# Kernel tuning notes

Measured on AMD Instinct MI355X. Metric: run time of the kernel, lower is better.

The kernel has to match this reference:

```python
import jax, jax.numpy as jnp
import numpy as np
from jax import lax

EPS = 1e-5

def _groupnorm1(v, scale, bias):
    # GroupNorm(1, C) on [bs, C] vectors (spatial dims are 1x1): normalize over C per sample
    m = jnp.mean(v, axis=-1, keepdims=True)
    var = jnp.mean((v - m) ** 2, axis=-1, keepdims=True)
    return (v - m) / jnp.sqrt(var + EPS) * scale + bias

def _mish(v):
    return v * jnp.tanh(jax.nn.softplus(v))


def setup_inputs() -> dict:
    key = jax.random.key(0)
    ks = jax.random.split(key, 5)
    bs, C, H, W = 32, 128, 64, 64
    K, red = 4, 16
    hid = C // red
    return {
        "x": jax.random.normal(ks[0], (bs, C, H, W), jnp.float32),
        "weight": jax.random.normal(ks[1], (K, C, C, 3, 3), jnp.float32) * 0.05,
        "bias": jax.random.normal(ks[2], (K, C), jnp.float32) * 0.05,
        "se_w1": jax.random.normal(ks[3], (hid, C), jnp.float32) * 0.1,
        "gn1_scale": jnp.ones((hid,), jnp.float32),
        "gn1_bias": jnp.zeros((hid,), jnp.float32),
        "se_w2": jax.random.normal(ks[4], (K, hid), jnp.float32) * 0.1,
        "gn2_scale": jnp.ones((K,), jnp.float32),
        "gn2_bias": jnp.zeros((K,), jnp.float32),
    }


def reference(x, weight, bias, se_w1, gn1_scale, gn1_bias, se_w2, gn2_scale, gn2_bias):
    bs, C, H, W = x.shape
    K, out_p, in_p, kh, kw = weight.shape

    # --- SqueezeAndExcitation attention -> [bs, K] in (0,1) ---
    pooled = jnp.mean(x, axis=(2, 3))                       # [bs, C]
    h1 = pooled @ se_w1.T                                   # [bs, hid] (1x1 conv, no bias)
    h1 = _mish(_groupnorm1(h1, gn1_scale, gn1_bias))
    h2 = h1 @ se_w2.T                                       # [bs, K]
    att = jax.nn.sigmoid(_groupnorm1(h2, gn2_scale, gn2_bias))

    # --- per-sample kernel / bias aggregation ---
    agg_w = jnp.einsum('bk,koihw->boihw', att, weight)      # [bs, out, in, kh, kw]
    agg_b = att @ bias                                      # [bs, out]

    # --- per-sample conv2d (equivalent to groups=bs grouped conv in torch) ---
    pad = ((1, 1), (1, 1))
    def per_sample(xi, wi):
        return lax.conv_general_dilated(
            xi[None], wi, window_strides=(1, 1), padding=pad,
            dimension_numbers=('NCHW', 'OIHW', 'NCHW'))[0]
    out = jax.vmap(per_sample)(x, agg_w)                    # [bs, out, H, W]
    return out + agg_b[:, :, None, None]
```

## Files before the change

### kernel.cpp

```cpp
#include <hip/hip_runtime.h>
#include <hip/hip_bf16.h>
#include <math.h>
#include <stdint.h>

#define EPS 1e-5f

typedef __attribute__((ext_vector_type(8))) short bf16x8;
typedef __attribute__((ext_vector_type(16))) float f32x16;

__device__ __forceinline__ ushort f2bf(float f) {
    union { float f; unsigned u; } v; v.f = f;
    unsigned r = (v.u + 0x7FFFu + ((v.u >> 16) & 1u)) >> 16;
    return (ushort)r;
}

__device__ __forceinline__ void dma16(const void* g, void* l) {
    __builtin_amdgcn_global_load_lds(
        (__attribute__((address_space(1))) const void*)(uintptr_t)g,
        (__attribute__((address_space(3))) void*)(uintptr_t)l,
        16, 0, 0);
}

__global__ __launch_bounds__(256) void transpose_kernel(const float* __restrict__ x,
                                                        ushort* __restrict__ xT,
                                                        float* __restrict__ partial) {
    __shared__ float T2[64][132];
    int bid = blockIdx.x;
    int b = (bid & 7) * 4 + (bid >> 9);
    int y = (bid >> 3) & 63;
    int t = threadIdx.x;

    int ic2 = t >> 1, half = t & 1;
    const float4* src = (const float4*)(x + (((size_t)b * 128 + ic2) * 64 + y) * 64 + half * 32);
    float s = 0.f;
#pragma unroll
    for (int i = 0; i < 8; ++i) {
        float4 v = src[i];
        int c0 = half * 32 + i * 4;
        T2[c0][ic2] = v.x; T2[c0 + 1][ic2] = v.y; T2[c0 + 2][ic2] = v.z; T2[c0 + 3][ic2] = v.w;
        s += v.x + v.y + v.z + v.w;
    }
    s += __shfl_xor(s, 1, 64);
    if (half == 0) partial[((size_t)b * 64 + y) * 128 + ic2] = s;
    __syncthreads();

    int col = t >> 2, icq = t & 3;
    const float4* row = (const float4*)&T2[col][icq * 32];
    uint pk[16];
#pragma unroll
    for (int m = 0; m < 8; ++m) {
        float4 v = row[m];
        pk[2 * m]     = (uint)f2bf(v.x) | ((uint)f2bf(v.y) << 16);
        pk[2 * m + 1] = (uint)f2bf(v.z) | ((uint)f2bf(v.w) << 16);
    }
    ushort* dst = xT + (((size_t)(b * 66 + y + 1)) * 66 + col + 1) * 128 + icq * 32;
    ((uint4*)dst)[0] = make_uint4(pk[0], pk[1], pk[2], pk[3]);
    ((uint4*)dst)[1] = make_uint4(pk[4], pk[5], pk[6], pk[7]);
    ((uint4*)dst)[2] = make_uint4(pk[8], pk[9], pk[10], pk[11]);
    ((uint4*)dst)[3] = make_uint4(pk[12], pk[13], pk[14], pk[15]);

    uint4 z = make_uint4(0, 0, 0, 0);
    if (y == 0) {
        uint4* row0 = (uint4*)(xT + ((size_t)b * 66 + 0) * 66 * 128);
        for (int i = t; i < 1056; i += 256) row0[i] = z;
    }
    if (y == 63) {
        uint4* row65 = (uint4*)(xT + ((size_t)b * 66 + 65) * 66 * 128);
        for (int i = t; i < 1056; i += 256) row65[i] = z;
    }
    if (t < 32) {
        int c = (t >> 4) * 65;
        int i = t & 15;
        *(uint4*)(xT + (((size_t)(b * 66 + y + 1)) * 66 + c) * 128 + i * 8) = z;
    }
}

__global__ __launch_bounds__(256) void sefuse_kernel(const float* __restrict__ partial,
                                                     const float* __restrict__ se_w1,
                                                     const float* __restrict__ gn1_s, const float* __restrict__ gn1_b,
                                                     const float* __restrict__ se_w2,
                                                     const float* __restrict__ gn2_s, const float* __restrict__ gn2_b,
                                                     float* __restrict__ att) {
    __shared__ float sA[256];
    __shared__ float pl[128];
    __shared__ float h1s[8];
    int b = blockIdx.x;
    int t = threadIdx.x;
    int ic = t & 127, hf = t >> 7;

    const float* p = partial + ((size_t)b * 64 + hf * 32) * 128 + ic;
    float s = 0.f;
#pragma unroll
    for (int k = 0; k < 32; ++k) s += p[k * 128];
    sA[t] = s;
    __syncthreads();
    if (t < 128) pl[t] = (sA[t] + sA[t + 128]) * (1.0f / 4096.0f);
    __syncthreads();
    if (t < 8) {
        float s1 = 0.f;
        for (int c = 0; c < 128; ++c) s1 += pl[c] * se_w1[t * 128 + c];
        h1s[t] = s1;
    }
    __syncthreads();
    if (t == 0) {
        float h1[8];
#pragma unroll
        for (int j = 0; j < 8; ++j) h1[j] = h1s[j];
        float m = 0.f;
#pragma unroll
        for (int j = 0; j < 8; ++j) m += h1[j];
        m *= 0.125f;
        float var = 0.f;
#pragma unroll
        for (int j = 0; j < 8; ++j) { float d = h1[j] - m; var += d * d; }
        var *= 0.125f;
        float inv = rsqrtf(var + EPS);
#pragma unroll
        for (int j = 0; j < 8; ++j) {
            float tt = (h1[j] - m) * inv * gn1_s[j] + gn1_b[j];
            float sp = (tt > 20.f) ? tt : log1pf(expf(tt));
            h1[j] = tt * tanhf(sp);
        }
        float h2[4];
#pragma unroll
        for (int k = 0; k < 4; ++k) {
            float s2 = 0.f;
#pragma unroll
            for (int j = 0; j < 8; ++j) s2 += h1[j] * se_w2[k * 8 + j];
            h2[k] = s2;
        }
        float m2 = 0.25f * (h2[0] + h2[1] + h2[2] + h2[3]);
        float v2 = 0.f;
#pragma unroll
        for (int k = 0; k < 4; ++k) { float d = h2[k] - m2; v2 += d * d; }
        v2 *= 0.25f;
        float inv2 = rsqrtf(v2 + EPS);
#pragma unroll
        for (int k = 0; k < 4; ++k) {
            float tt = (h2[k] - m2) * inv2 * gn2_s[k] + gn2_b[k];
            att[b * 4 + k] = 1.0f / (1.0f + expf(-tt));
        }
    }
}

__global__ __launch_bounds__(256) void aggw_kernel(const float* __restrict__ weight,
                                                   const float* __restrict__ att,
                                                   ushort* __restrict__ aggw) {
    int tq = (blockIdx.x % 72) * 256 + threadIdx.x;
    int rep = blockIdx.x / 72;
    int tap = tq >> 10;
    int within = tq & 1023;
    int oc = within >> 3;
    int p = within & 7;
    int g = (p - oc) & 7;
    int h = tap / 9, s = tap % 9;
    int ic0 = h * 64 + g * 8;

    float wv[4][8];
#pragma unroll
    for (int k = 0; k < 4; ++k)
#pragma unroll
        for (int j = 0; j < 8; ++j)
            wv[k][j] = weight[(((size_t)(k * 128 + oc)) * 128 + ic0 + j) * 9 + s];

    for (int b = rep * 8; b < rep * 8 + 8; ++b) {
        float a0 = att[b * 4 + 0], a1 = att[b * 4 + 1], a2 = att[b * 4 + 2], a3 = att[b * 4 + 3];
        uint pk[4];
#pragma unroll
        for (int q = 0; q < 4; ++q) {
            float f0 = a0 * wv[0][2 * q] + a1 * wv[1][2 * q] + a2 * wv[2][2 * q] + a3 * wv[3][2 * q];
            float f1 = a0 * wv[0][2 * q + 1] + a1 * wv[1][2 * q + 1] + a2 * wv[2][2 * q + 1] + a3 * wv[3][2 * q + 1];
            pk[q] = (uint)f2bf(f0) | ((uint)f2bf(f1) << 16);
        }
        *(uint4*)(aggw + (size_t)b * 147456 + (size_t)tq * 8) = make_uint4(pk[0], pk[1], pk[2], pk[3]);
    }
}

__global__ __launch_bounds__(512, 4) void conv_kernel(const ushort* __restrict__ xT,
                                                      const ushort* __restrict__ aggw,
                                                      const float* __restrict__ att,
                                                      const float* __restrict__ bias,
                                                      float* __restrict__ out) {
    __shared__ ushort ldsB[396 * 64];

    int bid = blockIdx.x;
    int xcd = bid & 7;
    int idx = bid >> 3;
    int b = xcd * 4 + (idx >> 4);
    int tile = idx & 15;
    int y0 = tile * 4;

    int tid = threadIdx.x;
    int l = tid & 63, w = tid >> 6;
    int wm = w & 1, wn = w >> 1;
    int l31 = l & 31, lhi = l >> 5;

    const ushort* xTb = xT + ((size_t)(b * 66 + y0)) * 66 * 128;
    const ushort* Asmp = aggw + (size_t)b * 147456;

    int ocofs[2], rotA[2];
#pragma unroll
    for (int mi = 0; mi < 2; ++mi) {
        int oc = wm * 64 + mi * 32 + l31;
        ocofs[mi] = oc * 64;
        rotA[mi] = (lhi + oc) & 7;
    }
    int CB[2];
#pragma unroll
    for (int ch = 0; ch < 2; ++ch) CB[ch] = wn * 66 + ch * 32 + l31;
    int rotB = (l31 + lhi) & 7;

    f32x16 acc[2][2];
#pragma unroll
    for (int mi = 0; mi < 2; ++mi)
#pragma unroll
        for (int ch = 0; ch < 2; ++ch)
#pragma unroll
            for (int q = 0; q < 16; ++q) acc[mi][ch][q] = 0.f;

    bf16x8 a[2][4];
#pragma unroll
    for (int mi = 0; mi < 2; ++mi)
#pragma unroll
        for (int icb = 0; icb < 4; ++icb)
            a[mi][icb] = *(const bf16x8*)(Asmp + ocofs[mi] + (((rotA[mi] + 2 * icb) & 7) << 3));

#pragma unroll
    for (int i = 0; i < 7; ++i) {
        int k = i * 512 + tid;
        if (k < 3168) {
            int rc = k >> 3;
            int c = rc % 66;
            int g = ((k & 7) - c) & 7;
            dma16(xTb + (size_t)rc * 128 + (g << 3), &ldsB[(size_t)k * 8]);
        }
    }
    __syncthreads();

    for (int hs = 0; hs < 18; ++hs) {
        int s = (hs >= 9) ? hs - 9 : hs;
        int kh = s / 3, kw = s - kh * 3;
        int celladd = kh * 66 + kw;
        const ushort* Anext = Asmp + (size_t)(hs + 1) * 8192;
#pragma unroll
        for (int icb = 0; icb < 4; ++icb) {
            int slotb = (rotB + 2 * icb + kw) & 7;
            bf16x8 bb[2];
#pragma unroll
            for (int ch = 0; ch < 2; ++ch) {
                int cell = CB[ch] + celladd;
                bb[ch] = *(const bf16x8*)&ldsB[(cell << 6) + (slotb << 3)];
            }
#pragma unroll
            for (int mi = 0; mi < 2; ++mi)
#pragma unroll
                for (int ch = 0; ch < 2; ++ch)
                    acc[mi][ch] = __builtin_amdgcn_mfma_f32_32x32x16_bf16(a[mi][icb], bb[ch], acc[mi][ch], 0, 0, 0);
            if (hs < 17) {
#pragma unroll
                for (int mi = 0; mi < 2; ++mi)
                    a[mi][icb] = *(const bf16x8*)(Anext + ocofs[mi] + (((rotA[mi] + 2 * icb) & 7) << 3));
            }
        }
        if (hs == 8) {
            __syncthreads();
#pragma unroll
            for (int i = 0; i < 7; ++i) {
                int k = i * 512 + tid;
                if (k < 3168) {
                    int rc = k >> 3;
                    int c = rc % 66;
                    int g = ((k & 7) - c) & 7;
                    dma16(xTb + (size_t)rc * 128 + 64 + (g << 3), &ldsB[(size_t)k * 8]);
                }
            }
            __syncthreads();
        }
    }

    float a0 = att[b * 4 + 0], a1 = att[b * 4 + 1], a2 = att[b * 4 + 2], a3 = att[b * 4 + 3];
    int y = y0 + wn;
#pragma unroll
    for (int mi = 0; mi < 2; ++mi)
#pragma unroll
        for (int q = 0; q < 16; ++q) {
            int oc = wm * 64 + mi * 32 + (q & 3) + 8 * (q >> 2) + 4 * lhi;
            float ab = a0 * bias[oc] + a1 * bias[128 + oc] + a2 * bias[256 + oc] + a3 * bias[384 + oc];
#pragma unroll
            for (int ch = 0; ch < 2; ++ch)
                out[(((size_t)b * 128 + oc) * 64 + y) * 64 + ch * 32 + l31] = acc[mi][ch][q] + ab;
        }
}

extern "C" void kernel_launch(void* const* d_in, const int* in_sizes, int n_in,
                              void* d_out, int out_size, void* d_ws, size_t ws_size,
                              hipStream_t stream) {
    const float* x      = (const float*)d_in[0];
    const float* weight = (const float*)d_in[1];
    const float* bias   = (const float*)d_in[2];
    const float* se_w1  = (const float*)d_in[3];
    const float* gn1_s  = (const float*)d_in[4];
    const float* gn1_b  = (const float*)d_in[5];
    const float* se_w2  = (const float*)d_in[6];
    const float* gn2_s  = (const float*)d_in[7];
    const float* gn2_b  = (const float*)d_in[8];
    float* out = (float*)d_out;

    float*  att     = (float*)((char*)d_ws + 16384);
    float*  partial = (float*)((char*)d_ws + 65536);
    ushort* aggw    = (ushort*)((char*)d_ws + 65536);
    ushort* xT      = (ushort*)((char*)d_ws + 10485760);

    transpose_kernel<<<2048, 256, 0, stream>>>(x, xT, partial);
    sefuse_kernel<<<32, 256, 0, stream>>>(partial, se_w1, gn1_s, gn1_b, se_w2, gn2_s, gn2_b, att);
    aggw_kernel<<<288, 256, 0, stream>>>(weight, att, aggw);
    conv_kernel<<<512, 512, 0, stream>>>(xT, aggw, att, bias, out);
}
```

Measured before the change: 105.0 us.

## Fuse SE path into aggregation kernel and enlarge conv tile to eight rows

Spatial pooling now uses atomic adds into a zeroed pooled buffer, replacing the per-row partial sums. Each aggregation block recomputes the squeeze-and-excitation attention for its eight samples, which removes the separate SE kernel launch. The conv kernel tile grows from four to eight output rows per block: each wave computes four N-subtiles instead of two, LDS use grows, and the grid halves to 256 blocks. In exchange this adds atomic contention, redundant SE computation and a memset, and the larger tile lowers occupancy and leaves fewer blocks than before to spread across CUs.

```diff
diff --git a/kernel.cpp b/kernel.cpp
--- a/kernel.cpp
+++ b/kernel.cpp
@@ -23,7 +23,7 @@
 
 __global__ __launch_bounds__(256) void transpose_kernel(const float* __restrict__ x,
                                                         ushort* __restrict__ xT,
-                                                        float* __restrict__ partial) {
+                                                        float* __restrict__ pooled) {
     __shared__ float T2[64][132];
     int bid = blockIdx.x;
     int b = (bid & 7) * 4 + (bid >> 9);
@@ -41,7 +41,7 @@
         s += v.x + v.y + v.z + v.w;
     }
     s += __shfl_xor(s, 1, 64);
-    if (half == 0) partial[((size_t)b * 64 + y) * 128 + ic2] = s;
+    if (half == 0) atomicAdd(&pooled[b * 128 + ic2], s * (1.0f / 4096.0f));
     __syncthreads();
 
     int col = t >> 2, icq = t & 3;
@@ -75,37 +75,39 @@
     }
 }
 
-__global__ __launch_bounds__(256) void sefuse_kernel(const float* __restrict__ partial,
-                                                     const float* __restrict__ se_w1,
-                                                     const float* __restrict__ gn1_s, const float* __restrict__ gn1_b,
-                                                     const float* __restrict__ se_w2,
-                                                     const float* __restrict__ gn2_s, const float* __restrict__ gn2_b,
-                                                     float* __restrict__ att) {
-    __shared__ float sA[256];
-    __shared__ float pl[128];
-    __shared__ float h1s[8];
-    int b = blockIdx.x;
+__global__ __launch_bounds__(256) void aggw_kernel(const float* __restrict__ weight,
+                                                   const float* __restrict__ pooled,
+                                                   const float* __restrict__ se_w1,
+                                                   const float* __restrict__ gn1_s, const float* __restrict__ gn1_b,
+                                                   const float* __restrict__ se_w2,
+                                                   const float* __restrict__ gn2_s, const float* __restrict__ gn2_b,
+                                                   float* __restrict__ att_out,
+                                                   ushort* __restrict__ aggw) {
+    __shared__ float pl[8][128];
+    __shared__ float h1s[8][8];
+    __shared__ float att_s[8][4];
+    int blk = blockIdx.x;
+    int rep = blk / 72;
     int t = threadIdx.x;
-    int ic = t & 127, hf = t >> 7;
-
-    const float* p = partial + ((size_t)b * 64 + hf * 32) * 128 + ic;
-    float s = 0.f;
-#pragma unroll
-    for (int k = 0; k < 32; ++k) s += p[k * 128];
-    sA[t] = s;
-    __syncthreads();
-    if (t < 128) pl[t] = (sA[t] + sA[t + 128]) * (1.0f / 4096.0f);
+
+#pragma unroll
+    for (int u = 0; u < 4; ++u) {
+        int pid = u * 256 + t;
+        int bl = pid >> 7, ic = pid & 127;
+        pl[bl][ic] = pooled[(rep * 8 + bl) * 128 + ic];
+    }
+    __syncthreads();
+    if (t < 64) {
+        int bl = t >> 3, jj = t & 7;
+        float s1 = 0.f;
+        for (int c = 0; c < 128; ++c) s1 += pl[bl][c] * se_w1[jj * 128 + c];
+        h1s[bl][jj] = s1;
+    }
     __syncthreads();
     if (t < 8) {
-        float s1 = 0.f;
-        for (int c = 0; c < 128; ++c) s1 += pl[c] * se_w1[t * 128 + c];
-        h1s[t] = s1;
-    }
-    __syncthreads();
-    if (t == 0) {
         float h1[8];
 #pragma unroll
-        for (int j = 0; j < 8; ++j) h1[j] = h1s[j];
+        for (int j = 0; j < 8; ++j) h1[j] = h1s[t][j];
         float m = 0.f;
 #pragma unroll
         for (int j = 0; j < 8; ++j) m += h1[j];
@@ -138,16 +140,14 @@
 #pragma unroll
         for (int k = 0; k < 4; ++k) {
             float tt = (h2[k] - m2) * inv2 * gn2_s[k] + gn2_b[k];
-            att[b * 4 + k] = 1.0f / (1.0f + expf(-tt));
-        }
-    }
-}
-
-__global__ __launch_bounds__(256) void aggw_kernel(const float* __restrict__ weight,
-                                                   const float* __restrict__ att,
-                                                   ushort* __restrict__ aggw) {
-    int tq = (blockIdx.x % 72) * 256 + threadIdx.x;
-    int rep = blockIdx.x / 72;
+            att_s[t][k] = 1.0f / (1.0f + expf(-tt));
+        }
+    }
+    __syncthreads();
+
+    if ((blk % 72) == 0 && t < 32) att_out[rep * 32 + t] = att_s[t >> 2][t & 3];
+
+    int tq = (blk % 72) * 256 + t;
     int tap = tq >> 10;
     int within = tq & 1023;
     int oc = within >> 3;
@@ -163,8 +163,10 @@
         for (int j = 0; j < 8; ++j)
             wv[k][j] = weight[(((size_t)(k * 128 + oc)) * 128 + ic0 + j) * 9 + s];
 
-    for (int b = rep * 8; b < rep * 8 + 8; ++b) {
-        float a0 = att[b * 4 + 0], a1 = att[b * 4 + 1], a2 = att[b * 4 + 2], a3 = att[b * 4 + 3];
+#pragma unroll
+    for (int bl = 0; bl < 8; ++bl) {
+        int b = rep * 8 + bl;
+        float a0 = att_s[bl][0], a1 = att_s[bl][1], a2 = att_s[bl][2], a3 = att_s[bl][3];
         uint pk[4];
 #pragma unroll
         for (int q = 0; q < 4; ++q) {
@@ -176,23 +178,23 @@
     }
 }
 
-__global__ __launch_bounds__(512, 4) void conv_kernel(const ushort* __restrict__ xT,
+__global__ __launch_bounds__(512, 2) void conv_kernel(const ushort* __restrict__ xT,
                                                       const ushort* __restrict__ aggw,
                                                       const float* __restrict__ att,
                                                       const float* __restrict__ bias,
                                                       float* __restrict__ out) {
-    __shared__ ushort ldsB[396 * 64];
+    __shared__ ushort ldsB[660 * 64];
 
     int bid = blockIdx.x;
     int xcd = bid & 7;
-    int idx = bid >> 3;
-    int b = xcd * 4 + (idx >> 4);
-    int tile = idx & 15;
-    int y0 = tile * 4;
+    int j = bid >> 3;
+    int b = xcd * 4 + (j >> 3);
+    int tile = j & 7;
+    int y0 = tile * 8;
 
     int tid = threadIdx.x;
     int l = tid & 63, w = tid >> 6;
-    int wm = w & 1, wn = w >> 1;
+    int wm = w >> 2, wn = w & 3;
     int l31 = l & 31, lhi = l >> 5;
 
     const ushort* xTb = xT + ((size_t)(b * 66 + y0)) * 66 * 128;
@@ -205,18 +207,19 @@
         ocofs[mi] = oc * 64;
         rotA[mi] = (lhi + oc) & 7;
     }
-    int CB[2];
-#pragma unroll
-    for (int ch = 0; ch < 2; ++ch) CB[ch] = wn * 66 + ch * 32 + l31;
+    int CB[4];
+#pragma unroll
+    for (int nb = 0; nb < 4; ++nb)
+        CB[nb] = (2 * wn + (nb >> 1)) * 66 + (nb & 1) * 32 + l31;
     int rotB = (l31 + lhi) & 7;
 
-    f32x16 acc[2][2];
+    f32x16 acc[2][4];
 #pragma unroll
     for (int mi = 0; mi < 2; ++mi)
 #pragma unroll
-        for (int ch = 0; ch < 2; ++ch)
-#pragma unroll
-            for (int q = 0; q < 16; ++q) acc[mi][ch][q] = 0.f;
+        for (int nb = 0; nb < 4; ++nb)
+#pragma unroll
+            for (int q = 0; q < 16; ++q) acc[mi][nb][q] = 0.f;
 
     bf16x8 a[2][4];
 #pragma unroll
@@ -226,9 +229,9 @@
             a[mi][icb] = *(const bf16x8*)(Asmp + ocofs[mi] + (((rotA[mi] + 2 * icb) & 7) << 3));
 
 #pragma unroll
-    for (int i = 0; i < 7; ++i) {
+    for (int i = 0; i < 11; ++i) {
         int k = i * 512 + tid;
-        if (k < 3168) {
+        if (k < 5280) {
             int rc = k >> 3;
             int c = rc % 66;
             int g = ((k & 7) - c) & 7;
@@ -245,17 +248,17 @@
 #pragma unroll
         for (int icb = 0; icb < 4; ++icb) {
             int slotb = (rotB + 2 * icb + kw) & 7;
-            bf16x8 bb[2];
-#pragma unroll
-            for (int ch = 0; ch < 2; ++ch) {
-                int cell = CB[ch] + celladd;
-                bb[ch] = *(const bf16x8*)&ldsB[(cell << 6) + (slotb << 3)];
+            bf16x8 bb[4];
+#pragma unroll
+            for (int nb = 0; nb < 4; ++nb) {
+                int cell = CB[nb] + celladd;
+                bb[nb] = *(const bf16x8*)&ldsB[(cell << 6) + (slotb << 3)];
             }
 #pragma unroll
             for (int mi = 0; mi < 2; ++mi)
 #pragma unroll
-                for (int ch = 0; ch < 2; ++ch)
-                    acc[mi][ch] = __builtin_amdgcn_mfma_f32_32x32x16_bf16(a[mi][icb], bb[ch], acc[mi][ch], 0, 0, 0);
+                for (int nb = 0; nb < 4; ++nb)
+                    acc[mi][nb] = __builtin_amdgcn_mfma_f32_32x32x16_bf16(a[mi][icb], bb[nb], acc[mi][nb], 0, 0, 0);
             if (hs < 17) {
 #pragma unroll
                 for (int mi = 0; mi < 2; ++mi)
@@ -265,9 +268,9 @@
         if (hs == 8) {
             __syncthreads();
 #pragma unroll
-            for (int i = 0; i < 7; ++i) {
+            for (int i = 0; i < 11; ++i) {
                 int k = i * 512 + tid;
-                if (k < 3168) {
+                if (k < 5280) {
                     int rc = k >> 3;
                     int c = rc % 66;
                     int g = ((k & 7) - c) & 7;
@@ -279,7 +282,6 @@
     }
 
     float a0 = att[b * 4 + 0], a1 = att[b * 4 + 1], a2 = att[b * 4 + 2], a3 = att[b * 4 + 3];
-    int y = y0 + wn;
 #pragma unroll
     for (int mi = 0; mi < 2; ++mi)
 #pragma unroll
@@ -287,8 +289,10 @@
             int oc = wm * 64 + mi * 32 + (q & 3) + 8 * (q >> 2) + 4 * lhi;
             float ab = a0 * bias[oc] + a1 * bias[128 + oc] + a2 * bias[256 + oc] + a3 * bias[384 + oc];
 #pragma unroll
-            for (int ch = 0; ch < 2; ++ch)
-                out[(((size_t)b * 128 + oc) * 64 + y) * 64 + ch * 32 + l31] = acc[mi][ch][q] + ab;
+            for (int nb = 0; nb < 4; ++nb) {
+                int y = y0 + 2 * wn + (nb >> 1);
+                out[(((size_t)b * 128 + oc) * 64 + y) * 64 + (nb & 1) * 32 + l31] = acc[mi][nb][q] + ab;
+            }
         }
 }
 
@@ -306,13 +310,14 @@
     const float* gn2_b  = (const float*)d_in[8];
     float* out = (float*)d_out;
 
-    float*  att     = (float*)((char*)d_ws + 16384);
-    float*  partial = (float*)((char*)d_ws + 65536);
-    ushort* aggw    = (ushort*)((char*)d_ws + 65536);
-    ushort* xT      = (ushort*)((char*)d_ws + 10485760);
-
-    transpose_kernel<<<2048, 256, 0, stream>>>(x, xT, partial);
-    sefuse_kernel<<<32, 256, 0, stream>>>(partial, se_w1, gn1_s, gn1_b, se_w2, gn2_s, gn2_b, att);
-    aggw_kernel<<<288, 256, 0, stream>>>(weight, att, aggw);
-    conv_kernel<<<512, 512, 0, stream>>>(xT, aggw, att, bias, out);
-}
+    float*  att    = (float*)d_ws;
+    float*  pooled = (float*)((char*)d_ws + 16384);
+    ushort* aggw   = (ushort*)((char*)d_ws + 65536);
+    ushort* xT     = (ushort*)((char*)d_ws + 10485760);
+
+    hipMemsetAsync(pooled, 0, 128 * 32 * sizeof(float), stream);
+    transpose_kernel<<<2048, 256, 0, stream>>>(x, xT, pooled);
+    aggw_kernel<<<288, 256, 0, stream>>>(weight, pooled, se_w1, gn1_s, gn1_b,
+                                         se_w2, gn2_s, gn2_b, att, aggw);
+    conv_kernel<<<256, 512, 0, stream>>>(xT, aggw, att, bias, out);
+}
```

Result: faster. 92.69 us (-11.7%).
